# Kernel optimization log

Measured on AMD Instinct MI355X. Metric: run time of the kernel, lower is better.

Reference implementation:

```python
import jax, jax.numpy as jnp
import numpy as np
import math

N_HEADS = 4
N_KV_GROUPS = 1
HEAD_DIM = 256
SLIDING_WINDOW = 512
ROPE_BASE = 1000000.0
EPS = 1e-6


def _rmsnorm(x, gamma):
    # normalize over last dim (head_dim), torch nn.RMSNorm semantics
    ms = jnp.mean(jnp.square(x), axis=-1, keepdims=True)
    return x * jax.lax.rsqrt(ms + EPS) * gamma


def _rope_tables(T, head_dim, dtype):
    inv_freq = 1.0 / (ROPE_BASE ** (jnp.arange(0, head_dim, 2, dtype=jnp.float32) / head_dim))
    t = jnp.arange(T, dtype=jnp.float32)
    freqs = jnp.outer(t, inv_freq)          # [T, head_dim/2]
    return jnp.cos(freqs).astype(dtype), jnp.sin(freqs).astype(dtype)


def _apply_rope(x, cos, sin):
    # x: [B, T, H, hd]; cos/sin: [T, hd/2] broadcast as [1, T, 1, hd/2]
    x0 = x[..., 0::2]
    x1 = x[..., 1::2]
    c = cos[None, :, None, :]
    s = sin[None, :, None, :]
    even = x0 * c - x1 * s
    odd = x0 * s + x1 * c
    return jnp.stack((even, odd), axis=-1).reshape(x.shape)


def setup_inputs() -> dict:
    key = jax.random.key(0)
    ks = jax.random.split(key, 5)
    B, T, C = 2, 4096, 1024
    scale = 0.02
    return {
        "x": jax.random.normal(ks[0], (B, T, C), dtype=jnp.float32),
        "Wq": jax.random.normal(ks[1], (C, C), dtype=jnp.float32) * scale,
        "Wk": jax.random.normal(ks[2], (N_KV_GROUPS * HEAD_DIM, C), dtype=jnp.float32) * scale,
        "Wv": jax.random.normal(ks[3], (N_KV_GROUPS * HEAD_DIM, C), dtype=jnp.float32) * scale,
        "Wo": jax.random.normal(ks[4], (C, C), dtype=jnp.float32) * scale,
        "q_gamma": jnp.ones((HEAD_DIM,), dtype=jnp.float32),
        "k_gamma": jnp.ones((HEAD_DIM,), dtype=jnp.float32),
    }


def reference(x, Wq, Wk, Wv, Wo, q_gamma, k_gamma):
    B, T, C = x.shape
    H, G, hd = N_HEADS, N_KV_GROUPS, HEAD_DIM
    rep = H // G

    q = (x @ Wq.T).reshape(B, T, H, hd)
    k = (x @ Wk.T).reshape(B, T, G, hd)
    v = (x @ Wv.T).reshape(B, T, G, hd)

    q = _rmsnorm(q, q_gamma)
    k = _rmsnorm(k, k_gamma)

    cos, sin = _rope_tables(T, hd, q.dtype)
    q = _apply_rope(q, cos, sin)
    k = _apply_rope(k, cos, sin)

    q = q.transpose(0, 2, 1, 3)                 # [B, H, T, hd]
    k = k.transpose(0, 2, 1, 3)                 # [B, G, T, hd]
    v = v.transpose(0, 2, 1, 3)
    k = jnp.repeat(k, rep, axis=1)              # [B, H, T, hd]
    v = jnp.repeat(v, rep, axis=1)

    scores = jnp.einsum("bhqd,bhkd->bhqk", q, k) / math.sqrt(hd)
    i = jnp.arange(T)[:, None]
    j = jnp.arange(T)[None, :]
    allowed = (j <= i) & (j >= i - SLIDING_WINDOW)   # causal sliding window
    scores = jnp.where(allowed, scores, -jnp.inf)
    attn = jax.nn.softmax(scores, axis=-1)
    out = jnp.einsum("bhqk,bhkd->bhqd", attn, v)     # [B, H, T, hd]
    out = out.transpose(0, 2, 1, 3).reshape(B, T, C)
    return out @ Wo.T
```

## Files before the change

### kernel.cpp

```cpp
#include <hip/hip_runtime.h>
#include <cstdint>
#include <cstddef>

#define T_SEQ 4096
#define NB    2
#define CDIM  1024
#define HD    256
#define NH    4

typedef __attribute__((ext_vector_type(8))) __bf16 bf16x8;
typedef __attribute__((ext_vector_type(4))) __bf16 bf16x4;
typedef __attribute__((ext_vector_type(4))) float  floatx4;

__device__ __forceinline__ floatx4 mfma16(bf16x8 a, bf16x8 b, floatx4 c) {
  return __builtin_amdgcn_mfma_f32_16x16x32_bf16(a, b, c, 0, 0, 0);
}

__device__ __forceinline__ void gl2lds16(const void* g, void* l) {
  __builtin_amdgcn_global_load_lds(
      (__attribute__((address_space(1))) void*)g,
      (__attribute__((address_space(3))) void*)l, 16, 0, 0);
}

__global__ __launch_bounds__(256) void cvt_all(const float* __restrict__ x,
                                               const float* __restrict__ wq,
                                               const float* __restrict__ wk,
                                               const float* __restrict__ wv,
                                               const float* __restrict__ wo,
                                               __bf16* __restrict__ xb,
                                               __bf16* __restrict__ wb,
                                               __bf16* __restrict__ wob) {
  int i = blockIdx.x * 256 + threadIdx.x;
  const float* src;
  __bf16* dst;
  int off;
  if (i < 2097152)      { src = x;  dst = xb;            off = i; }
  else if (i < 2359296) { src = wq; dst = wb;            off = i - 2097152; }
  else if (i < 2424832) { src = wk; dst = wb + 1048576;  off = i - 2359296; }
  else if (i < 2490368) { src = wv; dst = wb + 1310720;  off = i - 2424832; }
  else                  { src = wo; dst = wob;           off = i - 2490368; }
  float4 v = ((const float4*)src)[off];
  bf16x4 o;
  o[0] = (__bf16)v.x; o[1] = (__bf16)v.y; o[2] = (__bf16)v.z; o[3] = (__bf16)v.w;
  *(bf16x4*)&dst[(size_t)off * 4] = o;
}

template <typename OutT>
__global__ __launch_bounds__(256) void gemm_bt(const __bf16* __restrict__ A,
                                               const __bf16* __restrict__ B,
                                               OutT* __restrict__ C,
                                               int M, int N, int K) {
  __shared__ __bf16 As[128 * 64];
  __shared__ __bf16 Bs[128 * 64];
  const int tid  = threadIdx.x;
  const int lane = tid & 63;
  const int wave = tid >> 6;
  const int wm = wave >> 1, wn = wave & 1;
  const int lrow = lane & 15, quad = lane >> 4;
  const int bm = blockIdx.y, bn = blockIdx.x;

  const __bf16* gA = A + (size_t)(bm * 128) * K;
  const __bf16* gB = B + (size_t)(bn * 128) * K;
  const int arow = tid >> 3;
  const int acol = ((tid & 7) ^ ((tid >> 3) & 7)) * 8;
  const int l7 = lrow & 7;

  floatx4 acc[4][4] = {};

  for (int kt = 0; kt < K; kt += 64) {
#pragma unroll
    for (int i = 0; i < 4; ++i)
      gl2lds16(gA + (size_t)(i * 32 + arow) * K + kt + acol, &As[i * 2048 + tid * 8]);
#pragma unroll
    for (int i = 0; i < 4; ++i)
      gl2lds16(gB + (size_t)(i * 32 + arow) * K + kt + acol, &Bs[i * 2048 + tid * 8]);
    __syncthreads();
#pragma unroll
    for (int kk = 0; kk < 2; ++kk) {
      bf16x8 af[4], bfr[4];
#pragma unroll
      for (int mi = 0; mi < 4; ++mi)
        af[mi] = *(const bf16x8*)&As[(wm * 64 + mi * 16 + lrow) * 64 +
                                     ((kk * 4 + quad) ^ l7) * 8];
#pragma unroll
      for (int ni = 0; ni < 4; ++ni)
        bfr[ni] = *(const bf16x8*)&Bs[(wn * 64 + ni * 16 + lrow) * 64 +
                                      ((kk * 4 + quad) ^ l7) * 8];
#pragma unroll
      for (int mi = 0; mi < 4; ++mi)
#pragma unroll
        for (int ni = 0; ni < 4; ++ni)
          acc[mi][ni] = mfma16(af[mi], bfr[ni], acc[mi][ni]);
    }
    __syncthreads();
  }

  const int row0 = bm * 128 + wm * 64;
  const int col0 = bn * 128 + wn * 64;
#pragma unroll
  for (int mi = 0; mi < 4; ++mi)
#pragma unroll
    for (int ni = 0; ni < 4; ++ni)
#pragma unroll
      for (int r = 0; r < 4; ++r) {
        int row = row0 + mi * 16 + quad * 4 + r;
        int col = col0 + ni * 16 + lrow;
        C[(size_t)row * N + col] = (OutT)acc[mi][ni][r];
      }
}

__global__ __launch_bounds__(256) void rmsrope(const __bf16* __restrict__ qkv,
                                               const float* __restrict__ qg,
                                               const float* __restrict__ kg,
                                               __bf16* __restrict__ qr,
                                               __bf16* __restrict__ kr,
                                               __bf16* __restrict__ vt) {
  __shared__ __bf16 Ls[64 * 256];
  if (blockIdx.x >= 5120) {
    const int vb = blockIdx.x - 5120;
    const int b = vb >> 6, tt = vb & 63;
    const int tid = threadIdx.x;
    const __bf16* src = qkv + ((size_t)(b * 4096 + tt * 64)) * 1536 + 1280;
#pragma unroll
    for (int i = 0; i < 8; ++i)
      gl2lds16(src + (size_t)(i * 8 + (tid >> 5)) * 1536 + (tid & 31) * 8,
               &Ls[i * 2048 + tid * 8]);
    __syncthreads();
    __bf16 buf[64];
#pragma unroll
    for (int i = 0; i < 64; ++i) buf[i] = Ls[i * 256 + tid];
    __bf16* dst = vt + ((size_t)(b * 256 + tid)) * T_SEQ + tt * 64;
#pragma unroll
    for (int i = 0; i < 8; ++i)
      *(bf16x8*)&dst[i * 8] = *(const bf16x8*)&buf[i * 8];
    return;
  }

  const int inst = blockIdx.x * 4 + (threadIdx.x >> 6);
  const int lane = threadIdx.x & 63;
  const int rp = inst / 5, which = inst - rp * 5;
  const int row = rp * 2 + (lane >> 5);
  const int hl = lane & 31;
  const int b = row >> 12, t = row & 4095;

  const int srcoff = (which < 4) ? which * 256 : 1024;
  const __bf16* src = qkv + (size_t)row * 1536 + srcoff;
  bf16x8 xv = *(const bf16x8*)&src[hl * 8];

  float xf[8];
  float ss = 0.f;
#pragma unroll
  for (int j = 0; j < 8; ++j) { xf[j] = (float)xv[j]; ss += xf[j] * xf[j]; }
#pragma unroll
  for (int off = 16; off >= 1; off >>= 1) ss += __shfl_xor(ss, off);
  const float rms = rsqrtf(ss * (1.0f / 256.0f) + 1e-6f);

  const float* g = (which < 4) ? qg : kg;
  const float4 gv0 = *(const float4*)&g[hl * 8];
  const float4 gv1 = *(const float4*)&g[hl * 8 + 4];
  float y[8];
  y[0] = xf[0] * rms * gv0.x; y[1] = xf[1] * rms * gv0.y;
  y[2] = xf[2] * rms * gv0.z; y[3] = xf[3] * rms * gv0.w;
  y[4] = xf[4] * rms * gv1.x; y[5] = xf[5] * rms * gv1.y;
  y[6] = xf[6] * rms * gv1.z; y[7] = xf[7] * rms * gv1.w;

  const float c_log2 = -19.931568569324174f / 128.0f;
  bf16x8 ov;
#pragma unroll
  for (int j = 0; j < 4; ++j) {
    const int p = hl * 4 + j;
    const float a = (float)t * exp2f((float)p * c_log2);
    const float sn = __sinf(a), cs = __cosf(a);
    ov[2 * j]     = (__bf16)(y[2 * j] * cs - y[2 * j + 1] * sn);
    ov[2 * j + 1] = (__bf16)(y[2 * j] * sn + y[2 * j + 1] * cs);
  }

  __bf16* dst = (which < 4)
      ? qr + ((size_t)((b * NH + which) * T_SEQ) + t) * 256
      : kr + ((size_t)(b * T_SEQ) + t) * 256;
  *(bf16x8*)&dst[hl * 8] = ov;
}

__global__ __launch_bounds__(512, 4) void attn(const __bf16* __restrict__ qr,
                                               const __bf16* __restrict__ kr,
                                               const __bf16* __restrict__ vt,
                                               __bf16* __restrict__ ao) {
  __shared__ __bf16 Ks[2][32 * 256];
  __shared__ __bf16 Vs[2][256 * 32];
  __shared__ __bf16 Ps[2][64 * 32];

  const int bid = ((blockIdx.x & 7) << 6) | (blockIdx.x >> 3);
  const int qi = bid & 63, h = (bid >> 6) & 3, b = bid >> 8;
  const int tid = threadIdx.x, wave = tid >> 6, lane = tid & 63;
  const int wq = wave & 3;
  const int wk = wave >> 2;
  const int lrow = lane & 15, quad = lane >> 4;
  const int l7 = lrow & 7;

  const __bf16* Q = qr + (size_t)((b * NH + h) * T_SEQ) * 256;
  const __bf16* K = kr + (size_t)(b * T_SEQ) * 256;
  const __bf16* V = vt + (size_t)(b * 256) * T_SEQ;

  const int qbase = qi * 64;

  bf16x8 qf[8];
#pragma unroll
  for (int c = 0; c < 8; ++c)
    qf[c] = *(const bf16x8*)&Q[(size_t)(qbase + wq * 16 + lrow) * 256 +
                               c * 32 + quad * 8];

  bf16x8 onesv;
#pragma unroll
  for (int j = 0; j < 8; ++j) onesv[j] = (__bf16)1.0f;

  floatx4 o[8] = {};
  floatx4 lm = {};

  const int jt0 = (qi >= 8) ? 2 * qi - 16 : 0;
  const int jt1 = 2 * qi + 1;

  const int krow = tid >> 5;
  const int kcol = ((tid & 31) ^ (krow & 7)) * 8;
  const int vrow = tid >> 2;
  const int vcol = ((tid & 3) ^ ((vrow ^ (vrow >> 2)) & 3)) * 8;

#pragma unroll
  for (int i = 0; i < 2; ++i)
    gl2lds16(K + (size_t)(jt0 * 32 + i * 16 + krow) * 256 + kcol,
             &Ks[jt0 & 1][i * 4096 + tid * 8]);
#pragma unroll
  for (int i = 0; i < 2; ++i)
    gl2lds16(V + (size_t)(i * 128 + vrow) * T_SEQ + jt0 * 32 + vcol,
             &Vs[jt0 & 1][i * 4096 + tid * 8]);
#pragma unroll
  for (int i = 0; i < 2; ++i)
    gl2lds16(K + (size_t)((jt0 + 1) * 32 + i * 16 + krow) * 256 + kcol,
             &Ks[(jt0 + 1) & 1][i * 4096 + tid * 8]);

  for (int jt = jt0; jt <= jt1; ++jt) {
    if (jt < jt1) {
      asm volatile("s_waitcnt vmcnt(4)\n\ts_barrier" ::: "memory");
    } else {
      asm volatile("s_waitcnt vmcnt(2)\n\ts_barrier" ::: "memory");
    }

    const __bf16* Kb = Ks[jt & 1];

    floatx4 s = {};
    __builtin_amdgcn_s_setprio(1);
#pragma unroll
    for (int c = 0; c < 8; ++c) {
      bf16x8 kf = *(const bf16x8*)&Kb[(wk * 16 + lrow) * 256 +
                                      ((c * 4 + quad) ^ l7) * 8];
      s = mfma16(kf, qf[c], s);
    }
    __builtin_amdgcn_s_setprio(0);

    const bool full = (jt <= 2 * qi - 1) && (jt >= 2 * qi - 14);

    const float C1 = 0.09016844005556021f;
    const float C2 = 23.083120654223415f;
    __bf16* Pb = Ps[jt & 1];
    {
      bf16x4 pk;
#pragma unroll
      for (int r = 0; r < 4; ++r) {
        float v = s[r];
        if (!full) {
          const int jk = jt * 32 + wk * 16 + quad * 4 + r;
          const int iq = qbase + wq * 16 + lrow;
          v = ((jk <= iq) && (jk + 512 >= iq)) ? v : -1e30f;
        }
        pk[r] = (__bf16)exp2f(v * C1 - C2);
      }
      const int q = wq * 16 + lrow;
      const int chunk = (wk * 2 + (quad >> 1)) ^ ((q ^ (q >> 2)) & 3);
      *(bf16x4*)((char*)Pb + q * 64 + chunk * 16 + (quad & 1) * 8) = pk;
    }

    if (jt < jt1) {
      asm volatile("s_waitcnt lgkmcnt(0) vmcnt(2)\n\ts_barrier" ::: "memory");
    } else {
      asm volatile("s_waitcnt lgkmcnt(0) vmcnt(0)\n\ts_barrier" ::: "memory");
    }

    if (jt + 1 <= jt1) {
#pragma unroll
      for (int i = 0; i < 2; ++i)
        gl2lds16(V + (size_t)(i * 128 + vrow) * T_SEQ + (jt + 1) * 32 + vcol,
                 &Vs[(jt + 1) & 1][i * 4096 + tid * 8]);
    }
    if (jt + 2 <= jt1) {
#pragma unroll
      for (int i = 0; i < 2; ++i)
        gl2lds16(K + (size_t)((jt + 2) * 32 + i * 16 + krow) * 256 + kcol,
                 &Ks[jt & 1][i * 4096 + tid * 8]);
    }

    bf16x8 pf;
    {
      const int q = wq * 16 + lrow;
      pf = *(const bf16x8*)((char*)Pb + q * 64 +
                            (quad ^ ((q ^ (q >> 2)) & 3)) * 16);
    }

    __builtin_amdgcn_s_setprio(1);
    lm = mfma16(pf, onesv, lm);

    const __bf16* Vb = Vs[jt & 1];
#pragma unroll
    for (int n = 0; n < 8; ++n) {
      const int row = wk * 128 + n * 16 + lrow;
      bf16x8 vf = *(const bf16x8*)&Vb[row * 32 +
                                      ((quad ^ ((row ^ (row >> 2)) & 3)) * 8)];
      o[n] = mfma16(pf, vf, o[n]);
    }
    __builtin_amdgcn_s_setprio(0);
  }

#pragma unroll
  for (int r = 0; r < 4; ++r) {
    const float rl = 1.0f / lm[r];
    const int tg = qbase + wq * 16 + quad * 4 + r;
#pragma unroll
    for (int n = 0; n < 8; ++n)
      ao[((size_t)(b * T_SEQ + tg)) * CDIM + h * 256 + wk * 128 + n * 16 + lrow] =
          (__bf16)(o[n][r] * rl);
  }
}

extern "C" void kernel_launch(void* const* d_in, const int* in_sizes, int n_in,
                              void* d_out, int out_size, void* d_ws, size_t ws_size,
                              hipStream_t stream) {
  const float* x  = (const float*)d_in[0];
  const float* Wq = (const float*)d_in[1];
  const float* Wk = (const float*)d_in[2];
  const float* Wv = (const float*)d_in[3];
  const float* Wo = (const float*)d_in[4];
  const float* qg = (const float*)d_in[5];
  const float* kg = (const float*)d_in[6];
  float* out = (float*)d_out;

  const size_t M = (size_t)NB * T_SEQ;
  char* ws = (char*)d_ws;
  __bf16* xb  = (__bf16*)ws; ws += M * CDIM * 2;
  __bf16* wb  = (__bf16*)ws; ws += (size_t)1536 * CDIM * 2;
  __bf16* wob = (__bf16*)ws; ws += (size_t)CDIM * CDIM * 2;
  __bf16* qkv = (__bf16*)ws; ws += M * 1536 * 2;
  __bf16* qr  = (__bf16*)ws; ws += M * CDIM * 2;
  __bf16* kr  = (__bf16*)ws; ws += M * HD * 2;
  __bf16* vt  = (__bf16*)ws; ws += M * HD * 2;
  __bf16* ao  = (__bf16*)ws;

  cvt_all<<<10752, 256, 0, stream>>>(x, Wq, Wk, Wv, Wo, xb, wb, wob);

  gemm_bt<__bf16><<<dim3(12, 64), 256, 0, stream>>>(xb, wb, qkv, 8192, 1536, 1024);

  rmsrope<<<5248, 256, 0, stream>>>(qkv, qg, kg, qr, kr, vt);

  attn<<<NB * NH * (T_SEQ / 64), 512, 0, stream>>>(qr, kr, vt, ao);

  gemm_bt<float><<<dim3(8, 64), 256, 0, stream>>>(ao, wob, out, 8192, 1024, 1024);
}
```

Before: 208.6 us.

## Rewrite sliding-window attention with 32x32 MFMA, 128-query tiles and register-resident P

The attention kernel now uses 256-thread blocks that each cover 128 queries, with every wave owning 32 query rows. It runs 32x32x16 MFMAs over 64-key tiles instead of 16x16x32 MFMAs over 32-key tiles. The softmax probabilities stay in registers, repacked across half-waves with lane shuffles, rather than going through an LDS P buffer, which removes that LDS traffic and a barrier per tile. K/V double buffering now stages a whole 64-key tile per iteration with one barrier. The trade-off is fewer, heavier blocks (256 instead of 512) with much higher register and LDS use per block, so occupancy is lower.

```diff
diff --git a/kernel.cpp b/kernel.cpp
--- a/kernel.cpp
+++ b/kernel.cpp
@@ -11,9 +11,13 @@
 typedef __attribute__((ext_vector_type(8))) __bf16 bf16x8;
 typedef __attribute__((ext_vector_type(4))) __bf16 bf16x4;
 typedef __attribute__((ext_vector_type(4))) float  floatx4;
+typedef __attribute__((ext_vector_type(16))) float f32x16;
 
 __device__ __forceinline__ floatx4 mfma16(bf16x8 a, bf16x8 b, floatx4 c) {
   return __builtin_amdgcn_mfma_f32_16x16x32_bf16(a, b, c, 0, 0, 0);
+}
+__device__ __forceinline__ f32x16 mfma32(bf16x8 a, bf16x8 b, f32x16 c) {
+  return __builtin_amdgcn_mfma_f32_32x32x16_bf16(a, b, c, 0, 0, 0);
 }
 
 __device__ __forceinline__ void gl2lds16(const void* g, void* l) {
@@ -181,150 +185,151 @@
   *(bf16x8*)&dst[hl * 8] = ov;
 }
 
-__global__ __launch_bounds__(512, 4) void attn(const __bf16* __restrict__ qr,
+__global__ __launch_bounds__(256, 1) void attn(const __bf16* __restrict__ qr,
                                                const __bf16* __restrict__ kr,
                                                const __bf16* __restrict__ vt,
                                                __bf16* __restrict__ ao) {
-  __shared__ __bf16 Ks[2][32 * 256];
-  __shared__ __bf16 Vs[2][256 * 32];
-  __shared__ __bf16 Ps[2][64 * 32];
-
-  const int bid = ((blockIdx.x & 7) << 6) | (blockIdx.x >> 3);
-  const int qi = bid & 63, h = (bid >> 6) & 3, b = bid >> 8;
-  const int tid = threadIdx.x, wave = tid >> 6, lane = tid & 63;
-  const int wq = wave & 3;
-  const int wk = wave >> 2;
-  const int lrow = lane & 15, quad = lane >> 4;
-  const int l7 = lrow & 7;
+  __shared__ __bf16 Ks[2][64 * 256];
+  __shared__ __bf16 Vs[2][256 * 64];
+
+  const int bid = ((blockIdx.x & 7) << 5) | (blockIdx.x >> 3);
+  const int qi = bid & 31, h = (bid >> 5) & 3, b = bid >> 7;
+  const int tid = threadIdx.x, w = tid >> 6, lane = tid & 63;
+  const int l31 = lane & 31, hi = lane >> 5;
 
   const __bf16* Q = qr + (size_t)((b * NH + h) * T_SEQ) * 256;
   const __bf16* K = kr + (size_t)(b * T_SEQ) * 256;
   const __bf16* V = vt + (size_t)(b * 256) * T_SEQ;
 
-  const int qbase = qi * 64;
-
-  bf16x8 qf[8];
-#pragma unroll
-  for (int c = 0; c < 8; ++c)
-    qf[c] = *(const bf16x8*)&Q[(size_t)(qbase + wq * 16 + lrow) * 256 +
-                               c * 32 + quad * 8];
+  const int qbase = qi * 128;
+  const int qg = qbase + w * 32 + l31;
+  const int wt0 = (qi >= 4) ? 2 * qi - 8 : 0;
+  const int wt1 = 2 * qi + 1;
+
+  bf16x8 qf[16];
+#pragma unroll
+  for (int s = 0; s < 16; ++s)
+    qf[s] = *(const bf16x8*)&Q[(size_t)qg * 256 + s * 16 + hi * 8];
 
   bf16x8 onesv;
 #pragma unroll
   for (int j = 0; j < 8; ++j) onesv[j] = (__bf16)1.0f;
 
-  floatx4 o[8] = {};
-  floatx4 lm = {};
-
-  const int jt0 = (qi >= 8) ? 2 * qi - 16 : 0;
-  const int jt1 = 2 * qi + 1;
-
-  const int krow = tid >> 5;
-  const int kcol = ((tid & 31) ^ (krow & 7)) * 8;
-  const int vrow = tid >> 2;
-  const int vcol = ((tid & 3) ^ ((vrow ^ (vrow >> 2)) & 3)) * 8;
-
-#pragma unroll
-  for (int i = 0; i < 2; ++i)
-    gl2lds16(K + (size_t)(jt0 * 32 + i * 16 + krow) * 256 + kcol,
-             &Ks[jt0 & 1][i * 4096 + tid * 8]);
-#pragma unroll
-  for (int i = 0; i < 2; ++i)
-    gl2lds16(V + (size_t)(i * 128 + vrow) * T_SEQ + jt0 * 32 + vcol,
-             &Vs[jt0 & 1][i * 4096 + tid * 8]);
-#pragma unroll
-  for (int i = 0; i < 2; ++i)
-    gl2lds16(K + (size_t)((jt0 + 1) * 32 + i * 16 + krow) * 256 + kcol,
-             &Ks[(jt0 + 1) & 1][i * 4096 + tid * 8]);
-
-  for (int jt = jt0; jt <= jt1; ++jt) {
-    if (jt < jt1) {
-      asm volatile("s_waitcnt vmcnt(4)\n\ts_barrier" ::: "memory");
-    } else {
-      asm volatile("s_waitcnt vmcnt(2)\n\ts_barrier" ::: "memory");
-    }
-
-    const __bf16* Kb = Ks[jt & 1];
-
-    floatx4 s = {};
-    __builtin_amdgcn_s_setprio(1);
-#pragma unroll
-    for (int c = 0; c < 8; ++c) {
-      bf16x8 kf = *(const bf16x8*)&Kb[(wk * 16 + lrow) * 256 +
-                                      ((c * 4 + quad) ^ l7) * 8];
-      s = mfma16(kf, qf[c], s);
-    }
-    __builtin_amdgcn_s_setprio(0);
-
-    const bool full = (jt <= 2 * qi - 1) && (jt >= 2 * qi - 14);
-
-    const float C1 = 0.09016844005556021f;
-    const float C2 = 23.083120654223415f;
-    __bf16* Pb = Ps[jt & 1];
-    {
-      bf16x4 pk;
-#pragma unroll
-      for (int r = 0; r < 4; ++r) {
-        float v = s[r];
-        if (!full) {
-          const int jk = jt * 32 + wk * 16 + quad * 4 + r;
-          const int iq = qbase + wq * 16 + lrow;
-          v = ((jk <= iq) && (jk + 512 >= iq)) ? v : -1e30f;
+  f32x16 o[8] = {};
+  f32x16 lm = {};
+
+  const float C1 = 0.09016844005556021f;
+  const float C2 = 23.083120654223415f;
+
+#define STAGE_KV(WT)                                                          \
+  {                                                                           \
+    const int wt_ = (WT);                                                     \
+    __bf16* kd = Ks[wt_ & 1];                                                 \
+    __bf16* vd = Vs[wt_ & 1];                                                 \
+    _Pragma("unroll")                                                         \
+    for (int i = 0; i < 8; ++i) {                                             \
+      const int row = (w * 8 + i) * 2 + hi;                                   \
+      const int g = l31 ^ (row & 7);                                          \
+      gl2lds16(K + (size_t)(wt_ * 64 + row) * 256 + g * 8,                    \
+               kd + (w * 8 + i) * 512 + lane * 8);                            \
+    }                                                                         \
+    _Pragma("unroll")                                                         \
+    for (int i = 0; i < 8; ++i) {                                             \
+      const int row = (w * 8 + i) * 8 + (lane >> 3);                          \
+      const int g = (lane & 7) ^ (row & 7);                                   \
+      gl2lds16(V + (size_t)row * T_SEQ + wt_ * 64 + g * 8,                    \
+               vd + (w * 8 + i) * 512 + lane * 8);                            \
+    }                                                                         \
+  }
+
+  STAGE_KV(wt0);
+  asm volatile("s_waitcnt vmcnt(0)\n\ts_barrier" ::: "memory");
+
+  for (int wt = wt0; wt <= wt1; ++wt) {
+    if (wt < wt1) STAGE_KV(wt + 1);
+
+    const __bf16* Kb = Ks[wt & 1];
+    const __bf16* Vb = Vs[wt & 1];
+
+    f32x16 s0 = {}, s1 = {};
+#pragma unroll
+    for (int s = 0; s < 16; ++s) {
+      const int c = ((s * 2 + hi) ^ (l31 & 7)) * 8;
+      bf16x8 kf0 = *(const bf16x8*)&Kb[(l31) * 256 + c];
+      bf16x8 kf1 = *(const bf16x8*)&Kb[(32 + l31) * 256 + c];
+      s0 = mfma32(kf0, qf[s], s0);
+      s1 = mfma32(kf1, qf[s], s1);
+    }
+
+    const bool full = (wt <= 2 * qi - 1) && (wt >= 2 * qi - 6);
+    float p0[16], p1[16];
+#pragma unroll
+    for (int r = 0; r < 16; ++r) {
+      const int crow = (r & 3) + 8 * (r >> 2) + 4 * hi;
+      float v0 = s0[r], v1 = s1[r];
+      if (!full) {
+        const int k0 = wt * 64 + crow;
+        const int k1 = k0 + 32;
+        v0 = ((k0 <= qg) && (k0 + 512 >= qg)) ? v0 : -1e30f;
+        v1 = ((k1 <= qg) && (k1 + 512 >= qg)) ? v1 : -1e30f;
+      }
+      p0[r] = exp2f(v0 * C1 - C2);
+      p1[r] = exp2f(v1 * C1 - C2);
+    }
+
+    bf16x8 pa[2][2];
+#pragma unroll
+    for (int kt = 0; kt < 2; ++kt) {
+      const float* p = kt ? p1 : p0;
+#pragma unroll
+      for (int kh = 0; kh < 2; ++kh) {
+        unsigned X0, X1, Y0, Y1;
+        asm("v_cvt_pk_bf16_f32 %0, %1, %2" : "=v"(X0) : "v"(p[kh * 8 + 0]), "v"(p[kh * 8 + 1]));
+        asm("v_cvt_pk_bf16_f32 %0, %1, %2" : "=v"(X1) : "v"(p[kh * 8 + 2]), "v"(p[kh * 8 + 3]));
+        asm("v_cvt_pk_bf16_f32 %0, %1, %2" : "=v"(Y0) : "v"(p[kh * 8 + 4]), "v"(p[kh * 8 + 5]));
+        asm("v_cvt_pk_bf16_f32 %0, %1, %2" : "=v"(Y1) : "v"(p[kh * 8 + 6]), "v"(p[kh * 8 + 7]));
+        const unsigned pX0 = __shfl_xor(X0, 32), pX1 = __shfl_xor(X1, 32);
+        const unsigned pY0 = __shfl_xor(Y0, 32), pY1 = __shfl_xor(Y1, 32);
+        uint4 wv;
+        wv.x = hi ? pY0 : X0;
+        wv.y = hi ? pY1 : X1;
+        wv.z = hi ? Y0 : pX0;
+        wv.w = hi ? Y1 : pX1;
+        pa[kt][kh] = __builtin_bit_cast(bf16x8, wv);
+      }
+    }
+
+#pragma unroll
+    for (int kt = 0; kt < 2; ++kt)
+#pragma unroll
+      for (int kh = 0; kh < 2; ++kh)
+        lm = mfma32(pa[kt][kh], onesv, lm);
+
+#pragma unroll
+    for (int n = 0; n < 8; ++n) {
+      const int vrow = (n * 32 + l31) * 64;
+#pragma unroll
+      for (int kt = 0; kt < 2; ++kt)
+#pragma unroll
+        for (int kh = 0; kh < 2; ++kh) {
+          bf16x8 vf = *(const bf16x8*)&Vb[vrow +
+                                          (((kt * 4 + kh * 2 + hi) ^ (l31 & 7)) * 8)];
+          o[n] = mfma32(pa[kt][kh], vf, o[n]);
         }
-        pk[r] = (__bf16)exp2f(v * C1 - C2);
-      }
-      const int q = wq * 16 + lrow;
-      const int chunk = (wk * 2 + (quad >> 1)) ^ ((q ^ (q >> 2)) & 3);
-      *(bf16x4*)((char*)Pb + q * 64 + chunk * 16 + (quad & 1) * 8) = pk;
-    }
-
-    if (jt < jt1) {
-      asm volatile("s_waitcnt lgkmcnt(0) vmcnt(2)\n\ts_barrier" ::: "memory");
-    } else {
-      asm volatile("s_waitcnt lgkmcnt(0) vmcnt(0)\n\ts_barrier" ::: "memory");
-    }
-
-    if (jt + 1 <= jt1) {
-#pragma unroll
-      for (int i = 0; i < 2; ++i)
-        gl2lds16(V + (size_t)(i * 128 + vrow) * T_SEQ + (jt + 1) * 32 + vcol,
-                 &Vs[(jt + 1) & 1][i * 4096 + tid * 8]);
-    }
-    if (jt + 2 <= jt1) {
-#pragma unroll
-      for (int i = 0; i < 2; ++i)
-        gl2lds16(K + (size_t)((jt + 2) * 32 + i * 16 + krow) * 256 + kcol,
-                 &Ks[jt & 1][i * 4096 + tid * 8]);
-    }
-
-    bf16x8 pf;
-    {
-      const int q = wq * 16 + lrow;
-      pf = *(const bf16x8*)((char*)Pb + q * 64 +
-                            (quad ^ ((q ^ (q >> 2)) & 3)) * 16);
-    }
-
-    __builtin_amdgcn_s_setprio(1);
-    lm = mfma16(pf, onesv, lm);
-
-    const __bf16* Vb = Vs[jt & 1];
-#pragma unroll
-    for (int n = 0; n < 8; ++n) {
-      const int row = wk * 128 + n * 16 + lrow;
-      bf16x8 vf = *(const bf16x8*)&Vb[row * 32 +
-                                      ((quad ^ ((row ^ (row >> 2)) & 3)) * 8)];
-      o[n] = mfma16(pf, vf, o[n]);
-    }
-    __builtin_amdgcn_s_setprio(0);
-  }
-
-#pragma unroll
-  for (int r = 0; r < 4; ++r) {
+    }
+
+    if (wt < wt1)
+      asm volatile("s_waitcnt vmcnt(0) lgkmcnt(0)\n\ts_barrier" ::: "memory");
+  }
+#undef STAGE_KV
+
+#pragma unroll
+  for (int r = 0; r < 16; ++r) {
     const float rl = 1.0f / lm[r];
-    const int tg = qbase + wq * 16 + quad * 4 + r;
+    const int qrow = qbase + w * 32 + (r & 3) + 8 * (r >> 2) + 4 * hi;
 #pragma unroll
     for (int n = 0; n < 8; ++n)
-      ao[((size_t)(b * T_SEQ + tg)) * CDIM + h * 256 + wk * 128 + n * 16 + lrow] =
+      ao[((size_t)(b * T_SEQ + qrow)) * CDIM + h * 256 + n * 32 + l31] =
           (__bf16)(o[n][r] * rl);
   }
 }
@@ -358,7 +363,7 @@
 
   rmsrope<<<5248, 256, 0, stream>>>(qkv, qg, kg, qr, kr, vt);
 
-  attn<<<NB * NH * (T_SEQ / 64), 512, 0, stream>>>(qr, kr, vt, ao);
+  attn<<<NB * NH * (T_SEQ / 128), 256, 0, stream>>>(qr, kr, vt, ao);
 
   gemm_bt<float><<<dim3(8, 64), 256, 0, stream>>>(ao, wob, out, 8192, 1024, 1024);
 }
```

Result: slower. 220.8 us (+5.9%).
